# Kernel tuning notes

Measured on AMD Instinct MI355X. Metric: run time of the kernel, lower is better.

The kernel has to match this reference:

```python
import jax, jax.numpy as jnp
import numpy as np

B, S, D = 8, 2048, 1024
N = 256          # state_dim
H = 512          # selector_hidden
E = 8            # num_experts


def murmurhash3_finalizer(token_ids):
    # Torch code works in int64 but masks to 32 bits after each multiply and
    # values stay non-negative, so it is exactly uint32 wrapping arithmetic.
    x = token_ids.astype(jnp.uint32)
    x = x ^ (x >> 16)
    x = x * jnp.uint32(2246822507)
    x = x ^ (x >> 13)
    x = x * jnp.uint32(3266489909)
    x = x ^ (x >> 16)
    return x


def setup_inputs() -> dict:
    key = jax.random.key(0)
    ks = jax.random.split(key, 7)
    scale = 0.02
    return {
        "x": jax.random.normal(ks[0], (B, S, D), dtype=jnp.float32),
        "token_ids": jax.random.randint(ks[1], (B, S), 0, 50257, dtype=jnp.int32),
        "Win": jax.random.normal(ks[2], (E, N, D), dtype=jnp.float32) * scale,      # in_proj.weight per expert
        "Wsin": jax.random.normal(ks[3], (E, H, D), dtype=jnp.float32) * scale,     # selector_in.weight
        "Wsout": jax.random.normal(ks[4], (E, 4 * N, H), dtype=jnp.float32) * scale,  # selector_out.weight
        "Wout": jax.random.normal(ks[5], (E, D, N), dtype=jnp.float32) * scale,     # out_proj.weight
        "dparam": jnp.ones((E, N), dtype=jnp.float32),                              # per-expert d
    }


def _forward(x, Win, Wsin, Wsout, Wout, dparam, token_ids):
    b, s, d = x.shape
    e_num, n, _ = Win.shape
    routes = (murmurhash3_finalizer(token_ids) % jnp.uint32(e_num)).astype(jnp.int32)  # (B,S)

    # Per-token expert projections, selected by hash route (masked accumulation
    # over the small fixed expert count; honors per-token routing).
    u = jnp.zeros((b, s, n), x.dtype)
    a = jnp.zeros((b, s, n), x.dtype)
    bg = jnp.zeros((b, s, n), x.dtype)
    c = jnp.zeros((b, s, n), x.dtype)
    dg = jnp.zeros((b, s, n), x.dtype)
    for e in range(e_num):
        m = (routes == e)[..., None]
        u = jnp.where(m, jnp.einsum('bsd,nd->bsn', x, Win[e]), u)
        sh = jax.nn.silu(jnp.einsum('bsd,hd->bsh', x, Wsin[e]))
        sel = jnp.einsum('bsh,oh->bso', sh, Wsout[e])       # (B,S,4N)
        ar, br, cr, dr = jnp.split(sel, 4, axis=-1)
        a = jnp.where(m, jax.nn.sigmoid(ar), a)
        bg = jnp.where(m, jnp.tanh(br), bg)
        c = jnp.where(m, jnp.tanh(cr), c)
        dg = jnp.where(m, jax.nn.sigmoid(dr), dg)

    dvec = dparam[routes]              # (B,S,N) expert d param per token
    skip = dvec * dg * u               # residual term, state-independent

    bidx = jnp.arange(b)

    def step(states, inp):
        # states: (B,E,N) per-expert hidden state per batch row
        route_t, u_t, a_t, b_t, c_t, skip_t = inp
        h_prev = states[bidx, route_t]                 # (B,N)
        h = a_t * h_prev + b_t * u_t
        states = states.at[bidx, route_t].set(h)       # only routed expert updates
        y = c_t * h + skip_t
        return states, y

    xs = (routes.swapaxes(0, 1), u.swapaxes(0, 1), a.swapaxes(0, 1),
          bg.swapaxes(0, 1), c.swapaxes(0, 1), skip.swapaxes(0, 1))
    states0 = jnp.zeros((b, e_num, n), x.dtype)
    _, ys = jax.lax.scan(step, states0, xs)            # ys: (S,B,N)
    y = ys.swapaxes(0, 1)                              # (B,S,N)

    out = jnp.zeros((b, s, d), x.dtype)
    for e in range(e_num):
        m = (routes == e)[..., None]
        out = jnp.where(m, jnp.einsum('bsn,dn->bsd', y, Wout[e]), out)
    return out


def reference(x, token_ids, Win, Wsin, Wsout, Wout, dparam):
    return _forward(x, Win, Wsin, Wsout, Wout, dparam, token_ids)
```

## Files before the change

### kernel.cpp

```cpp
#include <hip/hip_runtime.h>


#define TOKS 16384
#define RPAD 16512
#define DD   1024
#define NN   256
#define HH   512
#define MAXTILES  136
#define MAXCHUNKS 576
#define CHUNK 32
#define CVTBLKS 12288

typedef short short8 __attribute__((ext_vector_type(8)));
typedef float floatx4 __attribute__((ext_vector_type(4)));
typedef _Float16 half_t;

#define AS_GLOBAL __attribute__((address_space(1)))
#define AS_LDS    __attribute__((address_space(3)))

__device__ __forceinline__ void gl_lds16(const void* g, void* l) {
    __builtin_amdgcn_global_load_lds((const AS_GLOBAL void*)g, (AS_LDS void*)l, 16, 0, 0);
}

__device__ __forceinline__ unsigned short f2bf(float f) {
    union { float f; unsigned u; } c; c.f = f;
    unsigned r = c.u + 0x7FFF + ((c.u >> 16) & 1);
    return (unsigned short)(r >> 16);
}
__device__ __forceinline__ int route_of(int token) {
    unsigned x = (unsigned)token;
    x ^= x >> 16; x *= 2246822507u; x ^= x >> 13; x *= 3266489909u; x ^= x >> 16;
    return (int)(x & 7u);
}
__device__ __forceinline__ float sigm(float v) { return 1.0f / (1.0f + __expf(-v)); }
__device__ __forceinline__ float ftanh(float v) {
    float e = __expf(2.0f * v);
    return 1.0f - 2.0f / (e + 1.0f);
}

__global__ void k_route(const int* __restrict__ tok, int* __restrict__ cnt) {
    int b = blockIdx.x, tid = threadIdx.x;
    __shared__ int lc[256 * 8];
    #pragma unroll
    for (int e = 0; e < 8; e++) lc[tid * 8 + e] = 0;
    #pragma unroll
    for (int i = 0; i < 8; i++) {
        int e = route_of(tok[b * 2048 + tid * 8 + i]);
        lc[tid * 8 + e]++;
    }
    __syncthreads();
    if (tid < 8) {
        int s = 0;
        for (int t = 0; t < 256; t++) s += lc[t * 8 + tid];
        cnt[b * 8 + tid] = s;
    }
}

__global__ void k_scatter(const int* __restrict__ tok, const int* __restrict__ cnt,
                          int* __restrict__ perm,
                          int* __restrict__ tileE, int* __restrict__ tileS,
                          int* __restrict__ tileR,
                          int* __restrict__ cGrp, int* __restrict__ cStart,
                          int* __restrict__ cLen, int* __restrict__ gBase,
                          int* __restrict__ meta,
                          const float* __restrict__ Win, const float* __restrict__ Wsin,
                          const float* __restrict__ Wsout, const float* __restrict__ Wout,
                          unsigned short* __restrict__ W12, unsigned short* __restrict__ Wso,
                          unsigned short* __restrict__ Wo) {
    int blk = blockIdx.x, tid = threadIdx.x;
    if (blk >= 8) {
        const int C12 = 8 * 768 * 1024 / 4, CSO = 8 * 1024 * 512 / 4;
        int c = (blk - 8) * 256 + tid;
        floatx4 v; unsigned short* dst;
        if (c < C12) {
            int d = c * 4;
            int e = d / (768 * 1024);
            int rem = d - e * (768 * 1024);
            int r = rem >> 10, k = rem & 1023;
            const float* src = (r < 256) ? (Win + (((size_t)e * 256 + r) << 10) + k)
                                         : (Wsin + (((size_t)e * 512 + (r - 256)) << 10) + k);
            v = __builtin_nontemporal_load((const floatx4*)src);
            dst = W12 + d;
        } else if (c < C12 + CSO) {
            int d = (c - C12) * 4;
            v = __builtin_nontemporal_load((const floatx4*)(Wsout + d));
            dst = Wso + d;
        } else {
            int d = (c - C12 - CSO) * 4;
            v = __builtin_nontemporal_load((const floatx4*)(Wout + d));
            dst = Wo + d;
        }
        ushort4 o;
        o.x = f2bf(v[0]); o.y = f2bf(v[1]); o.z = f2bf(v[2]); o.w = f2bf(v[3]);
        *(ushort4*)dst = o;
        return;
    }
    int b = blk;
    int lane = tid & 63, w = tid >> 6;
    __shared__ int sc[64], eoff[9], etile[9], gbs[65];
    __shared__ unsigned wsum[4][4];
    int r[8];
    int myc[8] = {0,0,0,0,0,0,0,0};
    #pragma unroll
    for (int i = 0; i < 8; i++) {
        int e = route_of(tok[b * 2048 + tid * 8 + i]);
        r[i] = e; myc[e]++;
    }
    if (tid < 64) sc[tid] = cnt[tid];
    __syncthreads();
    if (tid == 0) {
        int ce[8];
        for (int e = 0; e < 8; e++) {
            int s = 0;
            for (int b2 = 0; b2 < 8; b2++) s += sc[b2 * 8 + e];
            ce[e] = s;
        }
        eoff[0] = 0;
        for (int e = 0; e < 8; e++) eoff[e + 1] = eoff[e] + ce[e];
        if (b == 0) {
            etile[0] = 0;
            for (int e = 0; e < 8; e++) etile[e + 1] = etile[e] + (ce[e] + 127) / 128;
            meta[0] = etile[8];
            gbs[0] = 0;
            for (int g = 0; g < 64; g++) gbs[g + 1] = gbs[g] + (sc[g] + CHUNK - 1) / CHUNK;
            meta[1] = gbs[64];
        }
    }
    __syncthreads();
    unsigned p[4], v[4];
    #pragma unroll
    for (int k = 0; k < 4; k++) {
        p[k] = (unsigned)myc[2 * k] | ((unsigned)myc[2 * k + 1] << 16);
        v[k] = p[k];
    }
    #pragma unroll
    for (int off = 1; off < 64; off <<= 1) {
        #pragma unroll
        for (int k = 0; k < 4; k++) {
            unsigned o = __shfl_up(v[k], off, 64);
            if (lane >= off) v[k] += o;
        }
    }
    if (lane == 63) {
        #pragma unroll
        for (int k = 0; k < 4; k++) wsum[w][k] = v[k];
    }
    __syncthreads();
    unsigned add[4] = {0, 0, 0, 0};
    for (int ww = 0; ww < w; ww++)
        #pragma unroll
        for (int k = 0; k < 4; k++) add[k] += wsum[ww][k];
    int basep[8];
    #pragma unroll
    for (int e = 0; e < 8; e++) {
        int run = eoff[e];
        for (int b2 = 0; b2 < b; b2++) run += sc[b2 * 8 + e];
        unsigned ex = v[e >> 1] + add[e >> 1] - p[e >> 1];
        basep[e] = run + (int)((e & 1) ? (ex >> 16) : (ex & 0xffffu));
    }
    #pragma unroll
    for (int i = 0; i < 8; i++) {
        int e = r[i];
        perm[basep[e]++] = b * 2048 + tid * 8 + i;
    }
    if (b == 0) {
        if (tid < 8) {
            int e = tid, st = eoff[e], c = eoff[e + 1] - eoff[e], t0 = etile[e];
            for (int i = 0, k = 0; i < c; i += 128, k++) {
                tileE[t0 + k] = e; tileS[t0 + k] = st + i;
                tileR[t0 + k] = (c - i < 128) ? (c - i) : 128;
            }
        }
        if (tid < 64) {
            int g = tid, e = g & 7;
            int n = sc[g], base = gbs[g];
            int s0 = eoff[e];
            for (int b2 = 0; b2 < (g >> 3); b2++) s0 += sc[b2 * 8 + e];
            gBase[g] = base;
            for (int i = 0, c = 0; i < n; i += CHUNK, c++) {
                cGrp[base + c] = g;
                cStart[base + c] = s0 + i;
                cLen[base + c] = (n - i < CHUNK) ? (n - i) : CHUNK;
            }
        }
    }
}

__global__ void k_gather(const float* __restrict__ x, const int* __restrict__ perm,
                         unsigned short* __restrict__ Xs, unsigned short* __restrict__ SHb,
                         unsigned short* __restrict__ Yb) {
    int r = blockIdx.x, tid = threadIdx.x;
    if (r < TOKS) {
        int tok = perm[r];
        floatx4 v = __builtin_nontemporal_load(
            (const floatx4*)(x + (size_t)tok * 1024 + tid * 4));
        ushort4 o;
        o.x = f2bf(v[0]); o.y = f2bf(v[1]); o.z = f2bf(v[2]); o.w = f2bf(v[3]);
        *(ushort4*)(Xs + (size_t)r * 1024 + tid * 4) = o;
    } else {
        ushort4 z = {0, 0, 0, 0};
        *(ushort4*)(Xs + (size_t)r * 1024 + tid * 4) = z;
        if (tid < 128) *(ushort4*)(SHb + (size_t)r * 512 + tid * 4) = z;
        if (tid < 64)  *(ushort4*)(Yb + (size_t)r * 256 + tid * 4) = z;
    }
}

template<int MODE, int KD>
__global__ __launch_bounds__(256, 4)
void k_mfma(const unsigned short* __restrict__ A, const unsigned short* __restrict__ Bw,
            const int* __restrict__ perm, const float* __restrict__ dparam,
            half_t* __restrict__ Ub, unsigned short* __restrict__ SHb,
            half_t* __restrict__ Aa, half_t* __restrict__ Wg,
            half_t* __restrict__ Cc, half_t* __restrict__ Sk,
            float* __restrict__ out,
            const int* __restrict__ tileE, const int* __restrict__ tileS,
            const int* __restrict__ tileR, const int* __restrict__ meta) {
    const int mt = blockIdx.x;
    if (mt >= meta[0]) return;
    const int e = tileE[mt], pos0 = tileS[mt], rows = tileR[mt];
    const int col0 = blockIdx.y * 64;
    const int tid = threadIdx.x;
    const int w = tid >> 6, lane = tid & 63, quad = lane >> 4, l15 = lane & 15;
    const int wm = w & 1, wn = w >> 1;
    constexpr int NOUT = (MODE == 0) ? 768 : 1024;
    constexpr int NK = KD / 32;

    __shared__ unsigned short As[3][128 * 32];
    __shared__ unsigned short Bs[3][64 * 32];

    const int r0 = tid >> 2;
    const int c8s = ((tid & 3) ^ ((tid >> 3) & 3)) * 8;
    const unsigned short* ga = A + (size_t)(pos0 + r0) * KD + c8s;
    const unsigned short* gb = Bw + ((size_t)e * NOUT + col0 + r0) * KD + c8s;

    const int sq = (quad ^ ((l15 >> 1) & 3)) * 8;
    int aoff[4], boff[2];
    #pragma unroll
    for (int i = 0; i < 4; i++) aoff[i] = (wm * 64 + i * 16 + l15) * 32 + sq;
    #pragma unroll
    for (int j = 0; j < 2; j++) boff[j] = (wn * 32 + j * 16 + l15) * 32 + sq;

    floatx4 acc[4][2] = {};

    #define STAGE(buf, k0) do { \
        gl_lds16(ga + (k0),                    As[buf] + w * 512); \
        gl_lds16(ga + (size_t)64 * KD + (k0),  As[buf] + 2048 + w * 512); \
        gl_lds16(gb + (k0),                    Bs[buf] + w * 512); \
    } while (0)

    STAGE(0, 0);
    STAGE(1, 32);
    int cur = 0, pre = 2;
    for (int kt = 0; kt < NK; kt++) {
        if (kt < NK - 1) {
            asm volatile("s_waitcnt vmcnt(3)" ::: "memory");
        } else {
            asm volatile("s_waitcnt vmcnt(0)" ::: "memory");
        }
        __builtin_amdgcn_s_barrier();
        asm volatile("" ::: "memory");
        if (kt + 2 < NK) STAGE(pre, (kt + 2) * 32);
        short8 af[4], bf[2];
        #pragma unroll
        for (int i = 0; i < 4; i++) af[i] = *(const short8*)(As[cur] + aoff[i]);
        #pragma unroll
        for (int j = 0; j < 2; j++) bf[j] = *(const short8*)(Bs[cur] + boff[j]);
        __builtin_amdgcn_s_setprio(1);
        #pragma unroll
        for (int i = 0; i < 4; i++)
            #pragma unroll
            for (int j = 0; j < 2; j++)
                acc[i][j] = __builtin_amdgcn_mfma_f32_16x16x32_bf16(af[i], bf[j], acc[i][j], 0, 0, 0);
        __builtin_amdgcn_s_setprio(0);
        asm volatile("s_waitcnt lgkmcnt(0)" ::: "memory");
        __builtin_amdgcn_sched_barrier(0);
        cur = (cur == 2) ? 0 : cur + 1;
        pre = (pre == 2) ? 0 : pre + 1;
    }
    #undef STAGE
    asm volatile("" ::: "memory");

    #pragma unroll
    for (int i = 0; i < 4; i++) {
        #pragma unroll
        for (int r = 0; r < 4; r++) {
            int m = wm * 64 + i * 16 + quad * 4 + r;
            if (m >= rows) continue;
            size_t row = (size_t)(pos0 + m);
            if (MODE == 0) {
                if (col0 < 256) {
                    #pragma unroll
                    for (int j = 0; j < 2; j++) {
                        int n = col0 + wn * 32 + j * 16 + l15;
                        Ub[row * 256 + n] = (half_t)acc[i][j][r];
                    }
                } else {
                    #pragma unroll
                    for (int j = 0; j < 2; j++) {
                        int n = col0 - 256 + wn * 32 + j * 16 + l15;
                        float v = acc[i][j][r];
                        SHb[row * 512 + n] = f2bf(v * sigm(v));
                    }
                }
            } else if (MODE == 1) {
                int region = col0 >> 8;
                #pragma unroll
                for (int j = 0; j < 2; j++) {
                    int n0 = (col0 & 255) + wn * 32 + j * 16 + l15;
                    size_t idx = row * 256 + (size_t)n0;
                    float v = acc[i][j][r];
                    if (region == 0) {
                        Aa[idx] = (half_t)sigm(v);
                    } else if (region == 1) {
                        Wg[idx] = (half_t)(ftanh(v) * (float)Ub[idx]);
                    } else if (region == 2) {
                        Cc[idx] = (half_t)ftanh(v);
                    } else {
                        Sk[idx] = (half_t)(dparam[e * 256 + n0] * sigm(v) * (float)Ub[idx]);
                    }
                }
            } else {
                int tok = perm[row];
                #pragma unroll
                for (int j = 0; j < 2; j++) {
                    int n = col0 + wn * 32 + j * 16 + l15;
                    __builtin_nontemporal_store(acc[i][j][r], &out[(size_t)tok * 1024 + n]);
                }
            }
        }
    }
}

__global__ void k_scanA(const half_t* __restrict__ Aa, const half_t* __restrict__ Wg,
                        const int* __restrict__ cStart, const int* __restrict__ cLen,
                        const int* __restrict__ meta,
                        float* __restrict__ SA, float* __restrict__ SQ) {
    int id = blockIdx.x;
    if (id >= meta[1]) return;
    int t = threadIdx.x;
    int s0 = cStart[id], L = cLen[id];
    size_t idx = (size_t)s0 * 256 + t;
    float p = 1.0f, q = 0.0f;
    if (L == CHUNK) {
        #pragma unroll
        for (int i = 0; i < CHUNK; i++) {
            float a = (float)Aa[idx + (size_t)i * 256], ww = (float)Wg[idx + (size_t)i * 256];
            q = a * q + ww;
            p *= a;
        }
    } else {
        for (int i = 0; i < L; i++) {
            float a = (float)Aa[idx], ww = (float)Wg[idx];
            q = a * q + ww;
            p *= a;
            idx += 256;
        }
    }
    SA[(size_t)id * 256 + t] = p;
    SQ[(size_t)id * 256 + t] = q;
}

__global__ void k_scanC(const half_t* __restrict__ Aa, const half_t* __restrict__ Wg,
                        const half_t* __restrict__ Cc, const half_t* __restrict__ Sk,
                        const int* __restrict__ cGrp, const int* __restrict__ cStart,
                        const int* __restrict__ cLen, const int* __restrict__ gBase,
                        const float* __restrict__ SA, const float* __restrict__ SQ,
                        const int* __restrict__ meta,
                        unsigned short* __restrict__ Yb) {
    int id = blockIdx.x;
    if (id >= meta[1]) return;
    int t = threadIdx.x;
    int g = cGrp[id];
    int base = gBase[g];
    int c = id - base;
    float h = 0.0f;
    for (int j = 0; j < c; j++) {
        size_t k = (size_t)(base + j) * 256 + t;
        h = SA[k] * h + SQ[k];
    }
    int s0 = cStart[id], L = cLen[id];
    size_t idx = (size_t)s0 * 256 + t;
    if (L == CHUNK) {
        #pragma unroll
        for (int i = 0; i < CHUNK; i++) {
            size_t k = idx + (size_t)i * 256;
            float a = (float)Aa[k], ww = (float)Wg[k];
            float cc = (float)Cc[k], sk = (float)Sk[k];
            h = a * h + ww;
            Yb[k] = f2bf(cc * h + sk);
        }
    } else {
        for (int i = 0; i < L; i++) {
            float a = (float)Aa[idx], ww = (float)Wg[idx];
            float cc = (float)Cc[idx], sk = (float)Sk[idx];
            h = a * h + ww;
            Yb[idx] = f2bf(cc * h + sk);
            idx += 256;
        }
    }
}

extern "C" void kernel_launch(void* const* d_in, const int* in_sizes, int n_in,
                              void* d_out, int out_size, void* d_ws, size_t ws_size,
                              hipStream_t stream) {
    const float* xin   = (const float*)d_in[0];
    const int*   tok   = (const int*)d_in[1];
    const float* Win   = (const float*)d_in[2];
    const float* Wsin  = (const float*)d_in[3];
    const float* Wsout = (const float*)d_in[4];
    const float* Wout  = (const float*)d_in[5];
    const float* dpar  = (const float*)d_in[6];
    float* out = (float*)d_out;

    size_t off = 0;
    char* base = (char*)d_ws;
    auto alloc = [&](size_t bytes) -> void* {
        void* p = base + off;
        off += (bytes + 255) & ~(size_t)255;
        return p;
    };
    half_t*         Ub  = (half_t*)alloc((size_t)RPAD * NN * 2);
    unsigned short* SHb = (unsigned short*)alloc((size_t)RPAD * HH * 2);
    unsigned short* Xs  = (unsigned short*)alloc((size_t)RPAD * DD * 2);
    unsigned short* Yb  = (unsigned short*)alloc((size_t)RPAD * NN * 2);
    half_t* Aa = (half_t*)alloc((size_t)TOKS * NN * 2);
    half_t* Wg = (half_t*)alloc((size_t)TOKS * NN * 2);
    half_t* Cc = (half_t*)alloc((size_t)TOKS * NN * 2);
    half_t* Sk = (half_t*)alloc((size_t)TOKS * NN * 2);
    unsigned short* W12 = (unsigned short*)alloc((size_t)8 * 768 * 1024 * 2);
    unsigned short* Wso = (unsigned short*)alloc((size_t)8 * 1024 * 512 * 2);
    unsigned short* Wo  = (unsigned short*)alloc((size_t)8 * 1024 * 256 * 2);
    float* SA  = (float*)alloc((size_t)MAXCHUNKS * 256 * 4);
    float* SQ  = (float*)alloc((size_t)MAXCHUNKS * 256 * 4);
    int* perm   = (int*)alloc(TOKS * 4);
    int* cnt    = (int*)alloc(64 * 4);
    int* tileE  = (int*)alloc(MAXTILES * 4);
    int* tileS  = (int*)alloc(MAXTILES * 4);
    int* tileR  = (int*)alloc(MAXTILES * 4);
    int* cGrp   = (int*)alloc(MAXCHUNKS * 4);
    int* cStart = (int*)alloc(MAXCHUNKS * 4);
    int* cLen   = (int*)alloc(MAXCHUNKS * 4);
    int* gBase  = (int*)alloc(64 * 4);
    int* meta   = (int*)alloc(16 * 4);

    k_route<<<8, 256, 0, stream>>>(tok, cnt);
    k_scatter<<<8 + CVTBLKS, 256, 0, stream>>>(tok, cnt, perm, tileE, tileS, tileR,
                                               cGrp, cStart, cLen, gBase, meta,
                                               Win, Wsin, Wsout, Wout, W12, Wso, Wo);
    k_gather<<<RPAD, 256, 0, stream>>>(xin, perm, Xs, SHb, Yb);

    k_mfma<0, 1024><<<dim3(MAXTILES, 12), 256, 0, stream>>>(Xs, W12, perm, dpar,
        Ub, SHb, Aa, Wg, Cc, Sk, out, tileE, tileS, tileR, meta);
    k_mfma<1, 512><<<dim3(MAXTILES, 16), 256, 0, stream>>>(SHb, Wso, perm, dpar,
        Ub, SHb, Aa, Wg, Cc, Sk, out, tileE, tileS, tileR, meta);

    k_scanA<<<MAXCHUNKS, 256, 0, stream>>>(Aa, Wg, cStart, cLen, meta, SA, SQ);
    k_scanC<<<MAXCHUNKS, 256, 0, stream>>>(Aa, Wg, Cc, Sk, cGrp, cStart, cLen,
                                           gBase, SA, SQ, meta, Yb);

    k_mfma<2, 256><<<dim3(MAXTILES, 16), 256, 0, stream>>>(Yb, Wo, perm, dpar,
        Ub, SHb, Aa, Wg, Cc, Sk, out, tileE, tileS, tileR, meta);
}
```

Measured before the change: 318.4 us.

## Fuse chunked scan passes into one kernel with inter-block flag synchronization

Merges the two-pass chunked linear scan (chunk summaries, then carry propagation and output) into a single kernel. Each block publishes its chunk summary and raises a release flag. Later chunks in the same group spin on acquire loads of earlier flags before folding in the carries. This removes one kernel launch and the global barrier between passes. It depends on earlier blocks being scheduled before later ones; with 576 blocks the grid should fit on the device, but spin-waiting can still deadlock or stall if that ordering assumption fails.

```diff
diff --git a/kernel.cpp b/kernel.cpp
--- a/kernel.cpp
+++ b/kernel.cpp
@@ -38,9 +38,12 @@
     return 1.0f - 2.0f / (e + 1.0f);
 }
 
-__global__ void k_route(const int* __restrict__ tok, int* __restrict__ cnt) {
+__global__ void k_route(const int* __restrict__ tok, int* __restrict__ cnt,
+                        int* __restrict__ flags) {
     int b = blockIdx.x, tid = threadIdx.x;
     __shared__ int lc[256 * 8];
+    int f = b * 256 + tid;
+    if (f < MAXCHUNKS) flags[f] = 0;
     #pragma unroll
     for (int e = 0; e < 8; e++) lc[tid * 8 + e] = 0;
     #pragma unroll
@@ -331,24 +334,31 @@
     }
 }
 
-__global__ void k_scanA(const half_t* __restrict__ Aa, const half_t* __restrict__ Wg,
-                        const int* __restrict__ cStart, const int* __restrict__ cLen,
-                        const int* __restrict__ meta,
-                        float* __restrict__ SA, float* __restrict__ SQ) {
+__global__ void k_scan(const half_t* __restrict__ Aa, const half_t* __restrict__ Wg,
+                       const half_t* __restrict__ Cc, const half_t* __restrict__ Sk,
+                       const int* __restrict__ cGrp, const int* __restrict__ cStart,
+                       const int* __restrict__ cLen, const int* __restrict__ gBase,
+                       const int* __restrict__ meta,
+                       float* __restrict__ SA, float* __restrict__ SQ,
+                       int* __restrict__ flags,
+                       unsigned short* __restrict__ Yb) {
     int id = blockIdx.x;
     if (id >= meta[1]) return;
     int t = threadIdx.x;
+    int g = cGrp[id], base = gBase[g], c = id - base;
     int s0 = cStart[id], L = cLen[id];
-    size_t idx = (size_t)s0 * 256 + t;
+    size_t idx0 = (size_t)s0 * 256 + t;
     float p = 1.0f, q = 0.0f;
     if (L == CHUNK) {
         #pragma unroll
         for (int i = 0; i < CHUNK; i++) {
-            float a = (float)Aa[idx + (size_t)i * 256], ww = (float)Wg[idx + (size_t)i * 256];
+            size_t k = idx0 + (size_t)i * 256;
+            float a = (float)Aa[k], ww = (float)Wg[k];
             q = a * q + ww;
             p *= a;
         }
     } else {
+        size_t idx = idx0;
         for (int i = 0; i < L; i++) {
             float a = (float)Aa[idx], ww = (float)Wg[idx];
             q = a * q + ww;
@@ -358,38 +368,30 @@
     }
     SA[(size_t)id * 256 + t] = p;
     SQ[(size_t)id * 256 + t] = q;
-}
-
-__global__ void k_scanC(const half_t* __restrict__ Aa, const half_t* __restrict__ Wg,
-                        const half_t* __restrict__ Cc, const half_t* __restrict__ Sk,
-                        const int* __restrict__ cGrp, const int* __restrict__ cStart,
-                        const int* __restrict__ cLen, const int* __restrict__ gBase,
-                        const float* __restrict__ SA, const float* __restrict__ SQ,
-                        const int* __restrict__ meta,
-                        unsigned short* __restrict__ Yb) {
-    int id = blockIdx.x;
-    if (id >= meta[1]) return;
-    int t = threadIdx.x;
-    int g = cGrp[id];
-    int base = gBase[g];
-    int c = id - base;
+    __syncthreads();
+    if (t == 0) {
+        __threadfence();
+        __hip_atomic_store(&flags[id], 1, __ATOMIC_RELEASE, __HIP_MEMORY_SCOPE_AGENT);
+    }
     float h = 0.0f;
     for (int j = 0; j < c; j++) {
+        while (__hip_atomic_load(&flags[base + j], __ATOMIC_ACQUIRE,
+                                 __HIP_MEMORY_SCOPE_AGENT) == 0)
+            __builtin_amdgcn_s_sleep(8);
         size_t k = (size_t)(base + j) * 256 + t;
         h = SA[k] * h + SQ[k];
     }
-    int s0 = cStart[id], L = cLen[id];
-    size_t idx = (size_t)s0 * 256 + t;
     if (L == CHUNK) {
         #pragma unroll
         for (int i = 0; i < CHUNK; i++) {
-            size_t k = idx + (size_t)i * 256;
+            size_t k = idx0 + (size_t)i * 256;
             float a = (float)Aa[k], ww = (float)Wg[k];
             float cc = (float)Cc[k], sk = (float)Sk[k];
             h = a * h + ww;
             Yb[k] = f2bf(cc * h + sk);
         }
     } else {
+        size_t idx = idx0;
         for (int i = 0; i < L; i++) {
             float a = (float)Aa[idx], ww = (float)Wg[idx];
             float cc = (float)Cc[idx], sk = (float)Sk[idx];
@@ -442,8 +444,9 @@
     int* cLen   = (int*)alloc(MAXCHUNKS * 4);
     int* gBase  = (int*)alloc(64 * 4);
     int* meta   = (int*)alloc(16 * 4);
-
-    k_route<<<8, 256, 0, stream>>>(tok, cnt);
+    int* flags  = (int*)alloc(MAXCHUNKS * 4);
+
+    k_route<<<8, 256, 0, stream>>>(tok, cnt, flags);
     k_scatter<<<8 + CVTBLKS, 256, 0, stream>>>(tok, cnt, perm, tileE, tileS, tileR,
                                                cGrp, cStart, cLen, gBase, meta,
                                                Win, Wsin, Wsout, Wout, W12, Wso, Wo);
@@ -454,9 +457,8 @@
     k_mfma<1, 512><<<dim3(MAXTILES, 16), 256, 0, stream>>>(SHb, Wso, perm, dpar,
         Ub, SHb, Aa, Wg, Cc, Sk, out, tileE, tileS, tileR, meta);
 
-    k_scanA<<<MAXCHUNKS, 256, 0, stream>>>(Aa, Wg, cStart, cLen, meta, SA, SQ);
-    k_scanC<<<MAXCHUNKS, 256, 0, stream>>>(Aa, Wg, Cc, Sk, cGrp, cStart, cLen,
-                                           gBase, SA, SQ, meta, Yb);
+    k_scan<<<MAXCHUNKS, 256, 0, stream>>>(Aa, Wg, Cc, Sk, cGrp, cStart, cLen,
+                                          gBase, meta, SA, SQ, flags, Yb);
 
     k_mfma<2, 256><<<dim3(MAXTILES, 16), 256, 0, stream>>>(Yb, Wo, perm, dpar,
         Ub, SHb, Aa, Wg, Cc, Sk, out, tileE, tileS, tileR, meta);
```

After: 405.9 us. 1.27x slower.
